# Kernel optimization log

Measured on AMD Instinct MI355X. Metric: run time of the kernel, lower is better.

Reference implementation:

```python
import jax, jax.numpy as jnp
import numpy as np

N_NODES = 50000
N_EDGES = 800000
IN_DIM = 128
HID = 32
HEADS = 3
OUT_DIM = 128
NEG_SLOPE = 0.2  # PyG GATConv default leaky_relu slope
EPS = 1e-16


def setup_inputs() -> dict:
    key = jax.random.key(0)
    ks = jax.random.split(key, 16)
    x = jax.random.normal(ks[0], (N_NODES, IN_DIM), jnp.float32)
    edge_index = jax.random.randint(ks[1], (2, N_EDGES), 0, N_NODES, dtype=jnp.int32)
    s = 0.1
    return {
        'x': x,
        'edge_index': edge_index,
        # layer 1: in=128 -> heads=3, c=32, concat
        'W1': jax.random.normal(ks[2], (IN_DIM, HEADS * HID), jnp.float32) * s,
        'as1': jax.random.normal(ks[3], (HEADS, HID), jnp.float32) * s,
        'ad1': jax.random.normal(ks[4], (HEADS, HID), jnp.float32) * s,
        'b1': jnp.zeros((HEADS * HID,), jnp.float32),
        # layer 2: in=96 -> heads=3, c=32, concat
        'W2': jax.random.normal(ks[5], (HEADS * HID, HEADS * HID), jnp.float32) * s,
        'as2': jax.random.normal(ks[6], (HEADS, HID), jnp.float32) * s,
        'ad2': jax.random.normal(ks[7], (HEADS, HID), jnp.float32) * s,
        'b2': jnp.zeros((HEADS * HID,), jnp.float32),
        # layer 3: in=96 -> heads=1, c=128, mean (concat=False)
        'W3': jax.random.normal(ks[8], (HEADS * HID, OUT_DIM), jnp.float32) * s,
        'as3': jax.random.normal(ks[9], (1, OUT_DIM), jnp.float32) * s,
        'ad3': jax.random.normal(ks[10], (1, OUT_DIM), jnp.float32) * s,
        'b3': jnp.zeros((OUT_DIM,), jnp.float32),
    }


def _gat_layer(x, src, dst, W, a_s, a_d, b, concat):
    # x: [N, F_in]; src/dst: [E'] (self-loops already appended)
    n = x.shape[0]
    heads, c = a_s.shape
    h = (x @ W).reshape(n, heads, c)                      # [N, H, C]
    alpha_src = jnp.sum(h * a_s[None], axis=-1)           # [N, H]
    alpha_dst = jnp.sum(h * a_d[None], axis=-1)           # [N, H]
    e = jax.nn.leaky_relu(alpha_src[src] + alpha_dst[dst], NEG_SLOPE)  # [E', H]
    # segment softmax over incoming edges of each dst node
    m = jax.ops.segment_max(e, dst, num_segments=n)       # [N, H] (every node has a self-loop)
    e = jnp.exp(e - m[dst])
    denom = jax.ops.segment_sum(e, dst, num_segments=n)   # [N, H]
    alpha = e / (denom[dst] + EPS)                        # [E', H]
    # attention dropout: module is evaluated in inference mode -> identity
    out = jax.ops.segment_sum(alpha[:, :, None] * h[src], dst, num_segments=n)  # [N, H, C]
    out = out.reshape(n, heads * c) if concat else out.mean(axis=1)
    return out + b


def reference(x, edge_index, W1, as1, ad1, b1, W2, as2, ad2, b2, W3, as3, ad3, b3):
    n = x.shape[0]
    loops = jnp.arange(n, dtype=edge_index.dtype)
    src = jnp.concatenate([edge_index[0], loops])  # PyG add_self_loops=True
    dst = jnp.concatenate([edge_index[1], loops])
    h = _gat_layer(x, src, dst, W1, as1, ad1, b1, concat=True)
    h = jax.nn.elu(h)
    h = _gat_layer(h, src, dst, W2, as2, ad2, b2, concat=True)
    h = jax.nn.elu(h)
    out = _gat_layer(h, src, dst, W3, as3, ad3, b3, concat=False)
    return out
```

## Files before the change

kernel.cpp:

```cpp
#include <hip/hip_runtime.h>
#include <hip/hip_bf16.h>
#include <hip/hip_fp16.h>
#include <math.h>

#define N_NODES_C 50000
#define NBKT ((N_NODES_C + 255) / 256)
#define NEG_SLOPE 0.2f
#define EPS_ 1e-16f

typedef _Float16 f16x8 __attribute__((ext_vector_type(8)));
typedef float    f32x4 __attribute__((ext_vector_type(4)));

__device__ __forceinline__ float lrelu(float x){ return x > 0.f ? x : NEG_SLOPE * x; }

__global__ void cinit_k(int* __restrict__ counts, int n){
  int t = blockIdx.x * blockDim.x + threadIdx.x;
  if (t < n) counts[t] = 1;
}

__global__ void hist_k(const int* __restrict__ dstv, int* __restrict__ counts, int E){
  int t = blockIdx.x * blockDim.x + threadIdx.x;
  if (t < E) atomicAdd(&counts[dstv[t]], 1);
}

__global__ void chunksum_k(const int* __restrict__ counts, int* __restrict__ sums, int n){
  __shared__ int lds[4];
  int base = blockIdx.x * 1024;
  int t = threadIdx.x;
  int s = 0;
  for (int i = t; i < 1024; i += 256){ int idx = base + i; s += (idx < n) ? counts[idx] : 0; }
  for (int d = 32; d >= 1; d >>= 1) s += __shfl_xor(s, d);
  if ((t & 63) == 0) lds[t >> 6] = s;
  __syncthreads();
  if (t == 0) sums[blockIdx.x] = lds[0] + lds[1] + lds[2] + lds[3];
}

__global__ void scan_k(const int* __restrict__ counts, const int* __restrict__ csums,
                       int* __restrict__ row_ptr, int* __restrict__ bcur, int nch, int n){
  __shared__ int ws[16];
  __shared__ int boff;
  int base = blockIdx.x * 1024; int t = threadIdx.x; int idx = base + t;
  int v = (idx < n) ? counts[idx] : 0;
  int lane = t & 63, wid = t >> 6;
  int x = v;
  for (int d = 1; d < 64; d <<= 1){ int y = __shfl_up(x, d); if (lane >= d) x += y; }
  if (lane == 63) ws[wid] = x;
  if (t < 64){
    int c = (t < blockIdx.x) ? csums[t] : 0;
    for (int d = 32; d >= 1; d >>= 1) c += __shfl_xor(c, d);
    if (t == 0) boff = c;
  }
  __syncthreads();
  if (t < 16){ int y = ws[t]; for (int d = 1; d < 16; d <<= 1){ int z = __shfl_up(y, d); if (t >= d) y += z; } ws[t] = y; }
  __syncthreads();
  int excl = x - v + (wid ? ws[wid - 1] : 0) + boff;
  if (idx < n){
    row_ptr[idx] = excl;
    if ((idx & 255) == 0) bcur[idx >> 8] = excl;
  }
  if (blockIdx.x == nch - 1 && t == 0) row_ptr[n] = boff + ws[15];
}

__global__ void selfwrite_k(const int* __restrict__ row_ptr, int* __restrict__ esrc, int n){
  int v = blockIdx.x * blockDim.x + threadIdx.x;
  if (v < n) esrc[row_ptr[v]] = (int)(((unsigned)(v & 255) << 16) | (unsigned)v);
}

#define BATCH 2048
#define BCAP 32
__global__ __launch_bounds__(256) void bucket_k(const int* __restrict__ srcv, const int* __restrict__ dstv,
                                                int* __restrict__ bcur, unsigned* __restrict__ ebuf, int E){
  __shared__ unsigned stage[NBKT * BCAP];
  __shared__ int cnt[NBKT];
  int t = threadIdx.x;
  int start = blockIdx.x * BATCH;
  int end = start + BATCH; if (end > E) end = E;
  for (int i = t; i < NBKT; i += 256) cnt[i] = 0;
  __syncthreads();
  for (int e = start + t; e < end; e += 256){
    int s = srcv[e], d = dstv[e];
    int b = d >> 8;
    unsigned entry = (unsigned)s | ((unsigned)(d & 255) << 16);
    int pos = atomicAdd(&cnt[b], 1);
    if (pos < BCAP) stage[b * BCAP + pos] = entry;
    else { int p = atomicAdd(&bcur[b], 1); ebuf[p] = entry; }
  }
  __syncthreads();
  if (t < NBKT){
    int c = cnt[t]; if (c > BCAP) c = BCAP;
    if (c > 0){
      int p = atomicAdd(&bcur[t], c);
      for (int i = 0; i < c; i++) ebuf[p + i] = stage[t * BCAP + i];
    }
  }
}

__global__ __launch_bounds__(256) void bsort_k(const unsigned* __restrict__ ebuf,
                                               const int* __restrict__ row_ptr,
                                               int* __restrict__ esrc, int n){
  __shared__ int cnt[256];
  int b = blockIdx.x;
  int nb = b * 256;
  int t = threadIdx.x;
  cnt[t] = 1;
  __syncthreads();
  int hi_node = nb + 256; if (hi_node > n) hi_node = n;
  int beg = row_ptr[nb], end = row_ptr[hi_node];
  int realcnt = (end - beg) - (hi_node - nb);
  for (int i = beg + t; i < beg + realcnt; i += 256){
    unsigned e = ebuf[i];
    int dl = e >> 16;
    int rank = atomicAdd(&cnt[dl], 1);
    esrc[row_ptr[nb + dl] + rank] = (int)e;
  }
}

template<int K, int J>
__device__ void wpack_dev(const float* __restrict__ W, uint4* __restrict__ Wf, int blk, int nblk){
  constexpr int KS = K / 32, NT = J / 16;
  int tot = KS * NT * 64;
  for (int t = blk * 256 + threadIdx.x; t < tot; t += nblk * 256){
    int l = t & 63;
    int nt = (t >> 6) % NT;
    int kk = t / (64 * NT);
    int col = nt * 16 + (l & 15);
    int k0 = kk * 32 + (l >> 4) * 8;
    unsigned u[4];
    #pragma unroll
    for (int p = 0; p < 4; p++){
      __half2 h = __floats2half2_rn(W[(k0 + 2 * p) * J + col], W[(k0 + 2 * p + 1) * J + col]);
      u[p] = *reinterpret_cast<unsigned*>(&h);
    }
    uint4 v; v.x = u[0]; v.y = u[1]; v.z = u[2]; v.w = u[3];
    Wf[t] = v;
  }
}

__global__ void wpack_all_k(const float* W1, const float* W2, const float* W3,
                            uint4* Wf1, uint4* Wf2, uint4* Wf3){
  int b = blockIdx.x;
  if (b < 6) wpack_dev<128, 96>(W1, Wf1, b, 6);
  else if (b < 11) wpack_dev<96, 96>(W2, Wf2, b - 6, 5);
  else wpack_dev<96, 128>(W3, Wf3, b - 11, 6);
}

template<int K, int J, int HEADS, bool AF16>
__global__ __launch_bounds__(256) void gemm_mfma_k(
    const void* __restrict__ Ain, const uint4* __restrict__ Wf,
    const float* __restrict__ a_s, const float* __restrict__ a_d,
    __half* __restrict__ Hh, float* __restrict__ asrc, float* __restrict__ adst, int n){
  constexpr int KS = K / 32;
  constexpr int NT = J / 16;
  constexpr int CPR = K / 8;
  constexpr int NTPH = NT / HEADS;
  __shared__ uint4 Alds[64 * 16];
  int t = threadIdx.x;
  int rbase = blockIdx.x * 64;

  for (int i = t; i < 64 * CPR; i += 256){
    int r = i / CPR, c = i % CPR;
    int gr = rbase + r;
    uint4 v = make_uint4(0u, 0u, 0u, 0u);
    if (gr < n){
      if (AF16){
        v = ((const uint4*)Ain)[(size_t)gr * CPR + c];
      } else {
        const float4* af = (const float4*)Ain + (size_t)gr * (K / 4) + c * 2;
        float4 lo = af[0], hi = af[1];
        __half2 p0 = __floats2half2_rn(lo.x, lo.y);
        __half2 p1 = __floats2half2_rn(lo.z, lo.w);
        __half2 p2 = __floats2half2_rn(hi.x, hi.y);
        __half2 p3 = __floats2half2_rn(hi.z, hi.w);
        v.x = *reinterpret_cast<unsigned*>(&p0);
        v.y = *reinterpret_cast<unsigned*>(&p1);
        v.z = *reinterpret_cast<unsigned*>(&p2);
        v.w = *reinterpret_cast<unsigned*>(&p3);
      }
    }
    Alds[r * 16 + (c ^ (r & 7))] = v;
  }
  __syncthreads();

  int l = t & 63;
  int wrow = (t >> 6) * 16;
  int sub = l & 15;
  int lk = l >> 4;
  f32x4 acc[NT];
  #pragma unroll
  for (int i = 0; i < NT; i++) acc[i] = (f32x4){0.f, 0.f, 0.f, 0.f};

  for (int kk = 0; kk < KS; kk++){
    int trow = wrow + sub;
    int c = kk * 4 + lk;
    f16x8 a = *reinterpret_cast<const f16x8*>(&Alds[trow * 16 + (c ^ (trow & 7))]);
    const uint4* wb = Wf + (size_t)(kk * NT) * 64 + l;
    #pragma unroll
    for (int nt = 0; nt < NT; nt++){
      uint4 wv = wb[nt * 64];
      f16x8 bfr = *reinterpret_cast<const f16x8*>(&wv);
      acc[nt] = __builtin_amdgcn_mfma_f32_16x16x32_f16(a, bfr, acc[nt], 0, 0, 0);
    }
  }

  float ps[HEADS][4], pd[HEADS][4];
  #pragma unroll
  for (int h = 0; h < HEADS; h++)
    #pragma unroll
    for (int r = 0; r < 4; r++){ ps[h][r] = 0.f; pd[h][r] = 0.f; }
  #pragma unroll
  for (int nt = 0; nt < NT; nt++){
    int h = nt / NTPH;
    float sa = a_s[nt * 16 + sub];
    float sd = a_d[nt * 16 + sub];
    #pragma unroll
    for (int r = 0; r < 4; r++){ ps[h][r] += acc[nt][r] * sa; pd[h][r] += acc[nt][r] * sd; }
  }
  #pragma unroll
  for (int h = 0; h < HEADS; h++)
    #pragma unroll
    for (int r = 0; r < 4; r++)
      #pragma unroll
      for (int d = 1; d < 16; d <<= 1){
        ps[h][r] += __shfl_xor(ps[h][r], d);
        pd[h][r] += __shfl_xor(pd[h][r], d);
      }

  #pragma unroll
  for (int r = 0; r < 4; r++){
    int gr = rbase + wrow + lk * 4 + r;
    if (gr < n){
      #pragma unroll
      for (int nt = 0; nt < NT; nt++)
        Hh[(size_t)gr * J + nt * 16 + sub] = __float2half(acc[nt][r]);
    }
  }
  #pragma unroll
  for (int h = 0; h < HEADS; h++){
    if (sub == h){
      #pragma unroll
      for (int r = 0; r < 4; r++){
        int gr = rbase + wrow + lk * 4 + r;
        if (gr < n){
          asrc[gr * HEADS + h] = ps[h][r];
          adst[gr * HEADS + h] = pd[h][r];
        }
      }
    }
  }
}

template<int HEADS, int C, bool ELU, bool OUT16, int GN>
__global__ __launch_bounds__(256) void agg_k(const __half* __restrict__ Hh,
    const float* __restrict__ asrc, const float* __restrict__ adst,
    const int* __restrict__ row_ptr, const int* __restrict__ esrc,
    const float* __restrict__ bias, void* __restrict__ outv, int n){
  constexpr int J = HEADS * C;
  constexpr int NL = J / 2;
  int wid = blockIdx.x * (blockDim.x >> 6) + (threadIdx.x >> 6);
  int n0 = wid * GN;
  if (n0 >= n) return;
  int lane = threadIdx.x & 63;
  if (lane >= NL) return;
  int c0 = 2 * lane;
  int hh = c0 / C;
  const __half2* hp = (const __half2*)Hh;
  int gcnt = min(GN, n - n0);
  int rp = row_ptr[n0 + min(lane, gcnt)];
  float b0 = bias[c0], b1 = bias[c0 + 1];
  int bkt3 = (n0 & ~255) * HEADS;
  int e = __shfl(rp, 0);
  int eend = __shfl(rp, gcnt);
  int g = 0;
  int nb = __shfl(rp, 1);
  float acc0 = 0.f, acc1 = 0.f, den = 0.f;
  __half2* outh = (__half2*)outv;
  float* outf = (float*)outv;

  auto finalize = [&](int gg){
    float inv = 1.f / (den + EPS_);
    float r0 = acc0 * inv + b0, r1 = acc1 * inv + b1;
    if (ELU){
      r0 = r0 > 0.f ? r0 : __expf(r0) - 1.f;
      r1 = r1 > 0.f ? r1 : __expf(r1) - 1.f;
    }
    int node = n0 + gg;
    if (OUT16) outh[(size_t)node * NL + lane] = __floats2half2_rn(r0, r1);
    else *reinterpret_cast<float2*>(outf + (size_t)node * J + c0) = make_float2(r0, r1);
    acc0 = 0.f; acc1 = 0.f; den = 0.f;
  };

  for (; e + 8 <= eend; e += 8){
    int ev[8];
    #pragma unroll
    for (int u = 0; u < 8; u++) ev[u] = esrc[e + u];
    float w[8]; float2 f[8];
    #pragma unroll
    for (int u = 0; u < 8; u++){
      int s = ev[u] & 0xFFFF;
      int dl = ((unsigned)ev[u]) >> 16;
      float logit = asrc[s * HEADS + hh] + adst[bkt3 + dl * HEADS + hh];
      w[u] = __expf(lrelu(logit));
      f[u] = __half22float2(hp[(size_t)s * NL + lane]);
    }
    #pragma unroll
    for (int u = 0; u < 8; u++){
      while (e + u >= nb && g < gcnt - 1){ finalize(g); g++; nb = __shfl(rp, g + 1); }
      acc0 += w[u] * f[u].x; acc1 += w[u] * f[u].y; den += w[u];
    }
  }
  for (; e < eend; e++){
    int ev = esrc[e];
    int s = ev & 0xFFFF;
    int dl = ((unsigned)ev) >> 16;
    while (e >= nb && g < gcnt - 1){ finalize(g); g++; nb = __shfl(rp, g + 1); }
    float logit = asrc[s * HEADS + hh] + adst[bkt3 + dl * HEADS + hh];
    float wv = __expf(lrelu(logit));
    float2 f = __half22float2(hp[(size_t)s * NL + lane]);
    acc0 += wv * f.x; acc1 += wv * f.y; den += wv;
  }
  finalize(g);
}

extern "C" void kernel_launch(void* const* d_in, const int* in_sizes, int n_in,
                              void* d_out, int out_size, void* d_ws, size_t ws_size,
                              hipStream_t stream){
  const float* x   = (const float*)d_in[0];
  const int*   ei  = (const int*)  d_in[1];
  const float* W1  = (const float*)d_in[2];
  const float* as1 = (const float*)d_in[3];
  const float* ad1 = (const float*)d_in[4];
  const float* b1  = (const float*)d_in[5];
  const float* W2  = (const float*)d_in[6];
  const float* as2 = (const float*)d_in[7];
  const float* ad2 = (const float*)d_in[8];
  const float* b2  = (const float*)d_in[9];
  const float* W3  = (const float*)d_in[10];
  const float* as3 = (const float*)d_in[11];
  const float* ad3 = (const float*)d_in[12];
  const float* b3  = (const float*)d_in[13];
  float* out = (float*)d_out;

  const int N = N_NODES_C;
  const int E = in_sizes[1] / 2;
  const int* srcv = ei;
  const int* dstv = ei + E;

  char* ws = (char*)d_ws;
  auto alloc = [&](size_t bytes)->char*{ char* p = ws; ws += (bytes + 255) & ~(size_t)255; return p; };
  int*      counts  = (int*)     alloc((size_t)N * 4);
  int*      row_ptr = (int*)     alloc((size_t)(N + 1) * 4);
  int*      csums   = (int*)     alloc(64 * 4);
  int*      bcur    = (int*)     alloc(NBKT * 4);
  int*      esrc    = (int*)     alloc((size_t)(E + N) * 4);
  unsigned* ebuf    = (unsigned*)alloc((size_t)(E + N) * 4);
  __half*   Hh      = (__half*)  alloc((size_t)N * 128 * 2);
  __half*   feat_h  = (__half*)  alloc((size_t)N * 96 * 2);
  float*    a_src   = (float*)   alloc((size_t)N * 3 * 4);
  float*    a_dst   = (float*)   alloc((size_t)N * 3 * 4);
  uint4*    Wf1     = (uint4*)   alloc(128 * 96 * 2);
  uint4*    Wf2     = (uint4*)   alloc(96 * 96 * 2);
  uint4*    Wf3     = (uint4*)   alloc(96 * 128 * 2);

  cinit_k<<<(N + 255) / 256, 256, 0, stream>>>(counts, N);
  hist_k<<<(E + 255) / 256, 256, 0, stream>>>(dstv, counts, E);
  int nch = (N + 1023) / 1024;
  chunksum_k<<<nch, 256, 0, stream>>>(counts, csums, N);
  scan_k<<<nch, 1024, 0, stream>>>(counts, csums, row_ptr, bcur, nch, N);
  selfwrite_k<<<(N + 255) / 256, 256, 0, stream>>>(row_ptr, esrc, N);
  bucket_k<<<(E + BATCH - 1) / BATCH, 256, 0, stream>>>(srcv, dstv, bcur, ebuf, E);
  bsort_k<<<NBKT, 256, 0, stream>>>(ebuf, row_ptr, esrc, N);

  wpack_all_k<<<17, 256, 0, stream>>>(W1, W2, W3, Wf1, Wf2, Wf3);

  const int GN = 8;
  int gagg = ((N + GN - 1) / GN + 3) / 4;
  int ggemm = (N + 63) / 64;

  gemm_mfma_k<128, 96, 3, false><<<ggemm, 256, 0, stream>>>(x, Wf1, as1, ad1, Hh, a_src, a_dst, N);
  agg_k<3, 32, true, true, GN><<<gagg, 256, 0, stream>>>(Hh, a_src, a_dst, row_ptr, esrc, b1, feat_h, N);

  gemm_mfma_k<96, 96, 3, true><<<ggemm, 256, 0, stream>>>(feat_h, Wf2, as2, ad2, Hh, a_src, a_dst, N);
  agg_k<3, 32, true, true, GN><<<gagg, 256, 0, stream>>>(Hh, a_src, a_dst, row_ptr, esrc, b2, feat_h, N);

  gemm_mfma_k<96, 128, 1, true><<<ggemm, 256, 0, stream>>>(feat_h, Wf3, as3, ad3, Hh, a_src, a_dst, N);
  agg_k<1, 128, false, false, GN><<<gagg, 256, 0, stream>>>(Hh, a_src, a_dst, row_ptr, esrc, b3, out, N);
}
```

Before: 359.7 us.

## Aggregate one node per wavefront and drop packed dst index from edges

The aggregation kernel now assigns one destination node per 64-lane wavefront instead of a group of 8 nodes walked sequentially with boundary checks. The per-node dst logit is loaded once, and edges are processed in masked batches of 8. The edge array stores only the source index, so the packed dst-local bits are dropped. This removes the per-edge finalize/shuffle branching and the per-edge adst gather. In exchange it launches more waves and wastes lanes on short tails, since the average degree is about 17.

```diff
diff --git a/kernel.cpp b/kernel.cpp
--- a/kernel.cpp
+++ b/kernel.cpp
@@ -63,7 +63,7 @@
 
 __global__ void selfwrite_k(const int* __restrict__ row_ptr, int* __restrict__ esrc, int n){
   int v = blockIdx.x * blockDim.x + threadIdx.x;
-  if (v < n) esrc[row_ptr[v]] = (int)(((unsigned)(v & 255) << 16) | (unsigned)v);
+  if (v < n) esrc[row_ptr[v]] = v;
 }
 
 #define BATCH 2048
@@ -111,7 +111,7 @@
     unsigned e = ebuf[i];
     int dl = e >> 16;
     int rank = atomicAdd(&cnt[dl], 1);
-    esrc[row_ptr[nb + dl] + rank] = (int)e;
+    esrc[row_ptr[nb + dl] + rank] = (int)(e & 0xFFFFu);
   }
 }
 
@@ -249,76 +249,53 @@
   }
 }
 
-template<int HEADS, int C, bool ELU, bool OUT16, int GN>
+template<int HEADS, int C, bool ELU, bool OUT16>
 __global__ __launch_bounds__(256) void agg_k(const __half* __restrict__ Hh,
     const float* __restrict__ asrc, const float* __restrict__ adst,
     const int* __restrict__ row_ptr, const int* __restrict__ esrc,
     const float* __restrict__ bias, void* __restrict__ outv, int n){
   constexpr int J = HEADS * C;
   constexpr int NL = J / 2;
-  int wid = blockIdx.x * (blockDim.x >> 6) + (threadIdx.x >> 6);
-  int n0 = wid * GN;
-  if (n0 >= n) return;
+  int node = blockIdx.x * (blockDim.x >> 6) + (threadIdx.x >> 6);
+  if (node >= n) return;
   int lane = threadIdx.x & 63;
-  if (lane >= NL) return;
-  int c0 = 2 * lane;
+  bool colact = (NL == 64) || (lane < NL);
+  int cl = colact ? lane : (NL - 1);
+  int c0 = 2 * cl;
   int hh = c0 / C;
   const __half2* hp = (const __half2*)Hh;
-  int gcnt = min(GN, n - n0);
-  int rp = row_ptr[n0 + min(lane, gcnt)];
-  float b0 = bias[c0], b1 = bias[c0 + 1];
-  int bkt3 = (n0 & ~255) * HEADS;
-  int e = __shfl(rp, 0);
-  int eend = __shfl(rp, gcnt);
-  int g = 0;
-  int nb = __shfl(rp, 1);
+  float ad = adst[node * HEADS + hh];
+  int beg = row_ptr[node], end = row_ptr[node + 1];
   float acc0 = 0.f, acc1 = 0.f, den = 0.f;
-  __half2* outh = (__half2*)outv;
-  float* outf = (float*)outv;
-
-  auto finalize = [&](int gg){
+
+  for (int e0 = beg; e0 < end; e0 += 8){
+    int rem = end - e0;
+    int s[8];
+    #pragma unroll
+    for (int u = 0; u < 8; u++) s[u] = esrc[e0 + ((u < rem) ? u : (rem - 1))];
+    float wa[8];
+    #pragma unroll
+    for (int u = 0; u < 8; u++) wa[u] = asrc[s[u] * HEADS + hh];
+    float2 f[8];
+    #pragma unroll
+    for (int u = 0; u < 8; u++) f[u] = __half22float2(hp[(size_t)s[u] * NL + cl]);
+    #pragma unroll
+    for (int u = 0; u < 8; u++){
+      float wv = (u < rem) ? __expf(lrelu(wa[u] + ad)) : 0.f;
+      acc0 += wv * f[u].x; acc1 += wv * f[u].y; den += wv;
+    }
+  }
+  if (colact){
     float inv = 1.f / (den + EPS_);
-    float r0 = acc0 * inv + b0, r1 = acc1 * inv + b1;
+    float r0 = acc0 * inv + bias[c0];
+    float r1 = acc1 * inv + bias[c0 + 1];
     if (ELU){
       r0 = r0 > 0.f ? r0 : __expf(r0) - 1.f;
       r1 = r1 > 0.f ? r1 : __expf(r1) - 1.f;
     }
-    int node = n0 + gg;
-    if (OUT16) outh[(size_t)node * NL + lane] = __floats2half2_rn(r0, r1);
-    else *reinterpret_cast<float2*>(outf + (size_t)node * J + c0) = make_float2(r0, r1);
-    acc0 = 0.f; acc1 = 0.f; den = 0.f;
-  };
-
-  for (; e + 8 <= eend; e += 8){
-    int ev[8];
-    #pragma unroll
-    for (int u = 0; u < 8; u++) ev[u] = esrc[e + u];
-    float w[8]; float2 f[8];
-    #pragma unroll
-    for (int u = 0; u < 8; u++){
-      int s = ev[u] & 0xFFFF;
-      int dl = ((unsigned)ev[u]) >> 16;
-      float logit = asrc[s * HEADS + hh] + adst[bkt3 + dl * HEADS + hh];
-      w[u] = __expf(lrelu(logit));
-      f[u] = __half22float2(hp[(size_t)s * NL + lane]);
-    }
-    #pragma unroll
-    for (int u = 0; u < 8; u++){
-      while (e + u >= nb && g < gcnt - 1){ finalize(g); g++; nb = __shfl(rp, g + 1); }
-      acc0 += w[u] * f[u].x; acc1 += w[u] * f[u].y; den += w[u];
-    }
-  }
-  for (; e < eend; e++){
-    int ev = esrc[e];
-    int s = ev & 0xFFFF;
-    int dl = ((unsigned)ev) >> 16;
-    while (e >= nb && g < gcnt - 1){ finalize(g); g++; nb = __shfl(rp, g + 1); }
-    float logit = asrc[s * HEADS + hh] + adst[bkt3 + dl * HEADS + hh];
-    float wv = __expf(lrelu(logit));
-    float2 f = __half22float2(hp[(size_t)s * NL + lane]);
-    acc0 += wv * f.x; acc1 += wv * f.y; den += wv;
-  }
-  finalize(g);
+    if (OUT16) ((__half2*)outv)[(size_t)node * NL + cl] = __floats2half2_rn(r0, r1);
+    else *reinterpret_cast<float2*>((float*)outv + (size_t)node * J + c0) = make_float2(r0, r1);
+  }
 }
 
 extern "C" void kernel_launch(void* const* d_in, const int* in_sizes, int n_in,
@@ -372,16 +349,15 @@
 
   wpack_all_k<<<17, 256, 0, stream>>>(W1, W2, W3, Wf1, Wf2, Wf3);
 
-  const int GN = 8;
-  int gagg = ((N + GN - 1) / GN + 3) / 4;
-  int ggemm = (N + 63) / 64;
+  int gnode4 = (N + 3) / 4;
+  int ggemm  = (N + 63) / 64;
 
   gemm_mfma_k<128, 96, 3, false><<<ggemm, 256, 0, stream>>>(x, Wf1, as1, ad1, Hh, a_src, a_dst, N);
-  agg_k<3, 32, true, true, GN><<<gagg, 256, 0, stream>>>(Hh, a_src, a_dst, row_ptr, esrc, b1, feat_h, N);
+  agg_k<3, 32, true, true><<<gnode4, 256, 0, stream>>>(Hh, a_src, a_dst, row_ptr, esrc, b1, feat_h, N);
 
   gemm_mfma_k<96, 96, 3, true><<<ggemm, 256, 0, stream>>>(feat_h, Wf2, as2, ad2, Hh, a_src, a_dst, N);
-  agg_k<3, 32, true, true, GN><<<gagg, 256, 0, stream>>>(Hh, a_src, a_dst, row_ptr, esrc, b2, feat_h, N);
+  agg_k<3, 32, true, true><<<gnode4, 256, 0, stream>>>(Hh, a_src, a_dst, row_ptr, esrc, b2, feat_h, N);
 
   gemm_mfma_k<96, 128, 1, true><<<ggemm, 256, 0, stream>>>(feat_h, Wf3, as3, ad3, Hh, a_src, a_dst, N);
-  agg_k<1, 128, false, false, GN><<<gagg, 256, 0, stream>>>(Hh, a_src, a_dst, row_ptr, esrc, b3, out, N);
-}
+  agg_k<1, 128, false, false><<<gnode4, 256, 0, stream>>>(Hh, a_src, a_dst, row_ptr, esrc, b3, out, N);
+}
```

Result: faster. 329.7 us (-8.3%).
